# Performance work log

Measured on AMD Instinct MI355X. Metric: run time of the kernel, lower is better.

The kernel has to match this reference:

```python
import jax, jax.numpy as jnp
import numpy as np

B, T, D, H, L, V = 4, 1024, 1024, 16, 12, 8192
DH = D // H
FF = 4 * D


def _ln(x, g, b, eps=1e-5):
    m = x.mean(-1, keepdims=True)
    v = x.var(-1, keepdims=True)
    return (x - m) / jnp.sqrt(v + eps) * g + b


def setup_inputs() -> dict:
    key = jax.random.key(0)
    ks = iter(jax.random.split(key, 32))
    s = 0.02
    inp = {
        "idx": jax.random.randint(next(ks), (B, T), 0, V),
        "tk_emb": jax.random.normal(next(ks), (V, D), jnp.float32) * s,
        "pos_emb": jax.random.normal(next(ks), (V, D), jnp.float32) * s,
        "ln1_g": jnp.ones((L, D)), "ln1_b": jnp.zeros((L, D)),
        "Wq": jax.random.normal(next(ks), (L, H, D, DH), jnp.float32) * s,
        "bq": jnp.zeros((L, H, DH)),
        "Wk": jax.random.normal(next(ks), (L, H, D, DH), jnp.float32) * s,
        "bk": jnp.zeros((L, H, DH)),
        "Wv": jax.random.normal(next(ks), (L, H, D, DH), jnp.float32) * s,
        "bv": jnp.zeros((L, H, DH)),
        "Wo": jax.random.normal(next(ks), (L, D, D), jnp.float32) * s,
        "bo": jnp.zeros((L, D)),
        "ln2_g": jnp.ones((L, D)), "ln2_b": jnp.zeros((L, D)),
        "W1": jax.random.normal(next(ks), (L, D, FF), jnp.float32) * s,
        "b1": jnp.zeros((L, FF)),
        "W2": jax.random.normal(next(ks), (L, FF, D), jnp.float32) * s,
        "b2": jnp.zeros((L, D)),
        "lnf_g": jnp.ones((D,)), "lnf_b": jnp.zeros((D,)),
        "Wout": jax.random.normal(next(ks), (D, V), jnp.float32) * s,
        "bout": jnp.zeros((V,)),
    }
    return inp


def reference(idx, tk_emb, pos_emb, ln1_g, ln1_b, Wq, bq, Wk, bk, Wv, bv,
              Wo, bo, ln2_g, ln2_b, W1, b1, W2, b2, lnf_g, lnf_b, Wout, bout):
    b, t = idx.shape
    x = tk_emb[idx] + pos_emb[:t][None]          # [B,T,D]
    causal = jnp.tril(jnp.ones((t, t), bool))    # [T,T]
    scale = 1.0 / jnp.sqrt(jnp.asarray(DH, x.dtype))

    def block(x, p):
        g1, b1_, wq, bq_, wk, bk_, wv, bv_, wo, bo_, g2, b2_, w1, bb1, w2, bb2 = p
        h = _ln(x, g1, b1_)
        q = jnp.einsum('btd,hde->bhte', h, wq) + bq_[:, None, :]
        k = jnp.einsum('btd,hde->bhte', h, wk) + bk_[:, None, :]
        v = jnp.einsum('btd,hde->bhte', h, wv) + bv_[:, None, :]
        scores = jnp.einsum('bhte,bhse->bhts', q, k) * scale
        scores = jnp.where(causal, scores, jnp.asarray(-jnp.inf, scores.dtype))
        att = jax.nn.softmax(scores, axis=-1)
        o = jnp.einsum('bhts,bhse->bhte', att, v)              # [B,H,T,dh]
        o = o.transpose(0, 2, 1, 3).reshape(x.shape[0], x.shape[1], -1)
        x = x + o @ wo + bo_
        h2 = _ln(x, g2, b2_)
        x = x + jax.nn.gelu(h2 @ w1 + bb1, approximate=False) @ w2 + bb2
        return x, None

    layer_params = (ln1_g, ln1_b, Wq, bq, Wk, bk, Wv, bv, Wo, bo,
                    ln2_g, ln2_b, W1, b1, W2, b2)
    x, _ = jax.lax.scan(block, x, layer_params)
    x = _ln(x, lnf_g, lnf_b)
    logits = x @ Wout + bout
    return logits
```

## Files before the change

### kernel.cpp

```cpp
#include <hip/hip_runtime.h>

#define B_ 4
#define T_ 1024
#define D_ 1024
#define H_ 16
#define DH_ 64
#define L_ 12
#define FF_ 4096
#define V_ 8192
#define M_ 4096

typedef short bf16x8 __attribute__((ext_vector_type(8)));
typedef unsigned short u16x8 __attribute__((ext_vector_type(8)));
typedef unsigned short u16x4 __attribute__((ext_vector_type(4)));
typedef float f32x4 __attribute__((ext_vector_type(4)));

typedef const __attribute__((address_space(1))) void* gas1;
typedef __attribute__((address_space(3))) void* las3;
#define GL2LDS(g, l) __builtin_amdgcn_global_load_lds((gas1)(g), (las3)(l), 16, 0, 0)
#define MFMA16(a, b, c) __builtin_amdgcn_mfma_f32_16x16x32_bf16((a), (b), (c), 0, 0, 0)
#define WVM(n) asm volatile("s_waitcnt vmcnt(" #n ")" ::: "memory")
#define WLG() asm volatile("s_waitcnt lgkmcnt(0)" ::: "memory")
#define BARRIER() asm volatile("s_barrier" ::: "memory")

static __device__ __forceinline__ unsigned short f2bf(float f) {
  unsigned int u = __builtin_bit_cast(unsigned int, f);
  u += 0x7fffu + ((u >> 16) & 1u);
  return (unsigned short)(u >> 16);
}

static __device__ __forceinline__ void xcd_swz(int& bx, int& by) {
  const int gx = gridDim.x;
  const int id = by * gx + bx;
  const int q = (gx * gridDim.y) >> 3;
  const int nid = (id & 7) * q + (id >> 3);
  bx = nid % gx;
  by = nid / gx;
}

static __device__ __forceinline__ void ln_row_store(float4 r, const float* __restrict__ g,
                                                    const float* __restrict__ bb, int row,
                                                    int tid, float* red,
                                                    unsigned short* __restrict__ out) {
  float s = r.x + r.y + r.z + r.w;
  float s2 = r.x * r.x + r.y * r.y + r.z * r.z + r.w * r.w;
#pragma unroll
  for (int off = 32; off; off >>= 1) {
    s += __shfl_down(s, off);
    s2 += __shfl_down(s2, off);
  }
  if ((tid & 63) == 0) { red[tid >> 6] = s; red[4 + (tid >> 6)] = s2; }
  __syncthreads();
  const float ts = red[0] + red[1] + red[2] + red[3];
  const float ts2 = red[4] + red[5] + red[6] + red[7];
  const float mean = ts * (1.f / 1024.f);
  const float var = ts2 * (1.f / 1024.f) - mean * mean;
  const float rstd = rsqrtf(var + 1e-5f);
  const int c = tid * 4;
  u16x4 ov;
  ov[0] = f2bf((r.x - mean) * rstd * g[c] + bb[c]);
  ov[1] = f2bf((r.y - mean) * rstd * g[c + 1] + bb[c + 1]);
  ov[2] = f2bf((r.z - mean) * rstd * g[c + 2] + bb[c + 2]);
  ov[3] = f2bf((r.w - mean) * rstd * g[c + 3] + bb[c + 3]);
  *(u16x4*)&out[(size_t)row * D_ + c] = ov;
}

__global__ __launch_bounds__(256) void embed_ln_kernel(const int* __restrict__ idx,
                                                       const float* __restrict__ tk,
                                                       const float* __restrict__ pe,
                                                       const float* __restrict__ g,
                                                       const float* __restrict__ bb,
                                                       float* __restrict__ x,
                                                       unsigned short* __restrict__ out) {
  __shared__ float red[8];
  const int row = blockIdx.x, tid = threadIdx.x;
  const int t = row & (T_ - 1);
  const int id = idx[row];
  const int c = tid * 4;
  float4 a = *(const float4*)&tk[(size_t)id * D_ + c];
  const float4 p = *(const float4*)&pe[(size_t)t * D_ + c];
  a.x += p.x; a.y += p.y; a.z += p.z; a.w += p.w;
  *(float4*)&x[(size_t)row * D_ + c] = a;
  ln_row_store(a, g, bb, row, tid, red, out);
}

__global__ __launch_bounds__(256) void ln_kernel(const float* __restrict__ x,
                                                 const float* __restrict__ g,
                                                 const float* __restrict__ bb,
                                                 unsigned short* __restrict__ out) {
  __shared__ float red[8];
  const int row = blockIdx.x, tid = threadIdx.x;
  const float4 v = *(const float4*)&x[(size_t)row * D_ + tid * 4];
  ln_row_store(v, g, bb, row, tid, red, out);
}

__global__ __launch_bounds__(256) void redk_ln_kernel(const float* __restrict__ part,
                                                      const float* __restrict__ bias,
                                                      float* __restrict__ x,
                                                      const float* __restrict__ g,
                                                      const float* __restrict__ bb,
                                                      unsigned short* __restrict__ out) {
  __shared__ float red[8];
  const int row = blockIdx.x, tid = threadIdx.x;
  const size_t i = (size_t)row * D_ + tid * 4;
  float4 r = *(const float4*)&x[i];
  const float4 bv = *(const float4*)&bias[tid * 4];
  const size_t stride = (size_t)M_ * D_;
  float4 p0 = *(const float4*)&part[i];
  float4 p1 = *(const float4*)&part[i + stride];
  float4 p2 = *(const float4*)&part[i + 2 * stride];
  float4 p3 = *(const float4*)&part[i + 3 * stride];
  r.x += bv.x + ((p0.x + p1.x) + (p2.x + p3.x));
  r.y += bv.y + ((p0.y + p1.y) + (p2.y + p3.y));
  r.z += bv.z + ((p0.z + p1.z) + (p2.z + p3.z));
  r.w += bv.w + ((p0.w + p1.w) + (p2.w + p3.w));
  *(float4*)&x[i] = r;
  ln_row_store(r, g, bb, row, tid, red, out);
}

__global__ __launch_bounds__(256) void tpose_kernel(const float* __restrict__ in,
                                                    unsigned short* __restrict__ out,
                                                    int R, int C, long in_bs,
                                                    long out_bs_i, int inner, long out_bs_o) {
  __shared__ float tile[64][65];
  const int z = blockIdx.z;
  in += (long)z * in_bs;
  out += (long)(z % inner) * out_bs_i + (long)(z / inner) * out_bs_o;
  const int tx = threadIdx.x, ty = threadIdx.y;
  const int c = blockIdx.x * 64 + tx;
  const int r0 = blockIdx.y * 64;
#pragma unroll
  for (int i = 0; i < 16; i++) tile[ty + i * 4][tx] = in[(long)(r0 + ty + i * 4) * C + c];
  __syncthreads();
  const int oc = blockIdx.y * 64 + tx;
  const int or0 = blockIdx.x * 64;
#pragma unroll
  for (int i = 0; i < 16; i++)
    out[(long)(or0 + ty + i * 4) * R + oc] = f2bf(tile[tx][ty + i * 4]);
}

__global__ void bcat_kernel(const float* __restrict__ bq, const float* __restrict__ bk,
                            const float* __restrict__ bv, float* __restrict__ bqkv) {
  const int l = blockIdx.x;
  for (int i = threadIdx.x; i < 1024; i += 256) {
    bqkv[l * 3072 + i] = bq[l * 1024 + i];
    bqkv[l * 3072 + 1024 + i] = bk[l * 1024 + i];
    bqkv[l * 3072 + 2048 + i] = bv[l * 1024 + i];
  }
}

template <int EPI>
__global__ __launch_bounds__(512, 2) void gemm256(const unsigned short* __restrict__ A,
                                                  const unsigned short* __restrict__ Bt,
                                                  const float* __restrict__ bias,
                                                  void* outp, int Kc, int ld, int N) {
  __shared__ unsigned short lds[65536];
  const int tid = threadIdx.x;
  const int lane = tid & 63, w = tid >> 6;
  const int wm = w >> 2, wn = w & 3;
  const int l15 = lane & 15, lh = lane >> 4;
  int bx = blockIdx.x, by = blockIdx.y;
  xcd_swz(bx, by);
  const int row0 = by * 256, col0 = bx * 256;
  const int z = blockIdx.z;
  const int nt = Kc >> 6;
  const int laneoff = (lh * 8) ^ (((l15 >> 1) & 3) << 3);
  const int cswz = ((tid & 3) * 8) ^ (((tid >> 3) & 3) << 3);
  const unsigned short* gA = A + (size_t)(row0 + (tid >> 2)) * ld + z * Kc + cswz;
  const unsigned short* gB = Bt + (size_t)(col0 + (tid >> 2)) * ld + z * Kc + cswz;
  const size_t rblk = (size_t)128 * ld;
  const int arow = wm * 128 + l15;
  const int brow = wn * 64 + l15;

  f32x4 acc[8][4];
#pragma unroll
  for (int m = 0; m < 8; m++)
#pragma unroll
    for (int n = 0; n < 4; n++) acc[m][n] = f32x4{0.f, 0.f, 0.f, 0.f};

  auto issueA = [&](int t, int r) {
    unsigned short* d = lds + (t & 1) * 32768 + r * 8192 + tid * 8;
    const unsigned short* s = gA + t * 64 + r * 32;
    GL2LDS(s, d);
    GL2LDS(s + rblk, d + 4096);
  };
  auto issueB = [&](int t, int r) {
    unsigned short* d = lds + (t & 1) * 32768 + 16384 + r * 8192 + tid * 8;
    const unsigned short* s = gB + t * 64 + r * 32;
    GL2LDS(s, d);
    GL2LDS(s + rblk, d + 4096);
  };

  issueA(0, 0); issueB(0, 0); issueA(0, 1); issueB(0, 1);
  issueA(1, 0); issueB(1, 0);
  WVM(8);
  BARRIER();

  bf16x8 aF[4], bF[4];
  for (int t = 0; t < nt; ++t) {
    const bool last = (t == nt - 1);
    const unsigned short* ab = lds + (t & 1) * 32768;
    const unsigned short* bb2 = ab + 16384;
#pragma unroll
    for (int m = 0; m < 4; m++) aF[m] = *(const bf16x8*)(ab + (arow + m * 16) * 32 + laneoff);
#pragma unroll
    for (int n = 0; n < 4; n++) bF[n] = *(const bf16x8*)(bb2 + (brow + n * 16) * 32 + laneoff);
    if (!last) issueA(t + 1, 1);
    BARRIER();
    __builtin_amdgcn_s_setprio(1);
#pragma unroll
    for (int m = 0; m < 4; m++)
#pragma unroll
      for (int n = 0; n < 4; n++) acc[m][n] = MFMA16(aF[m], bF[n], acc[m][n]);
    __builtin_amdgcn_s_setprio(0);
    BARRIER();
#pragma unroll
    for (int m = 0; m < 4; m++) aF[m] = *(const bf16x8*)(ab + (arow + (m + 4) * 16) * 32 + laneoff);
    if (!last) issueB(t + 1, 1);
    BARRIER();
    __builtin_amdgcn_s_setprio(1);
#pragma unroll
    for (int m = 0; m < 4; m++)
#pragma unroll
      for (int n = 0; n < 4; n++) acc[m + 4][n] = MFMA16(aF[m], bF[n], acc[m + 4][n]);
    __builtin_amdgcn_s_setprio(0);
    if (last) { WVM(0); } else { WVM(8); }
    BARRIER();
#pragma unroll
    for (int m = 0; m < 4; m++) aF[m] = *(const bf16x8*)(ab + 8192 + (arow + m * 16) * 32 + laneoff);
#pragma unroll
    for (int n = 0; n < 4; n++) bF[n] = *(const bf16x8*)(bb2 + 8192 + (brow + n * 16) * 32 + laneoff);
    if (t + 2 < nt) issueA(t + 2, 0);
    BARRIER();
    __builtin_amdgcn_s_setprio(1);
#pragma unroll
    for (int m = 0; m < 4; m++)
#pragma unroll
      for (int n = 0; n < 4; n++) acc[m][n] = MFMA16(aF[m], bF[n], acc[m][n]);
    __builtin_amdgcn_s_setprio(0);
    BARRIER();
#pragma unroll
    for (int m = 0; m < 4; m++) aF[m] = *(const bf16x8*)(ab + 8192 + (arow + (m + 4) * 16) * 32 + laneoff);
    if (t + 2 < nt) issueB(t + 2, 0);
    BARRIER();
    __builtin_amdgcn_s_setprio(1);
#pragma unroll
    for (int m = 0; m < 4; m++)
#pragma unroll
      for (int n = 0; n < 4; n++) acc[m + 4][n] = MFMA16(aF[m], bF[n], acc[m + 4][n]);
    __builtin_amdgcn_s_setprio(0);
    if (!last) {
      if (t == nt - 2) { WVM(4); } else { WVM(8); }
    }
    BARRIER();
  }

#pragma unroll
  for (int n = 0; n < 4; n++) {
    const int c = col0 + wn * 64 + n * 16 + l15;
    const float bv = (EPI == 4) ? 0.f : bias[c];
#pragma unroll
    for (int m = 0; m < 8; m++) {
      const int r = row0 + wm * 128 + m * 16 + lh * 4;
#pragma unroll
      for (int j = 0; j < 4; j++) {
        float val = acc[m][n][j] + bv;
        const size_t oi = (size_t)(r + j) * N + c;
        if constexpr (EPI == 0) {
          ((unsigned short*)outp)[oi] = f2bf(val);
        } else if constexpr (EPI == 1) {
          val = 0.5f * val * (1.f + erff(val * 0.70710678118654752f));
          ((unsigned short*)outp)[oi] = f2bf(val);
        } else if constexpr (EPI == 4) {
          ((float*)outp)[(size_t)z * ((size_t)gridDim.y * 256) * N + oi] = val;
        } else {
          ((float*)outp)[oi] = val;
        }
      }
    }
  }
}

template <int EPI, int BN, int DEPTH>
__global__ __launch_bounds__(256) void gemmP(const unsigned short* __restrict__ A,
                                             const unsigned short* __restrict__ Bt,
                                             const float* __restrict__ bias,
                                             const float* resid, void* outp,
                                             int K, int N) {
  constexpr int NB = DEPTH + 1;
  constexpr int TILE = (128 + BN) * 32;
  constexpr int NF = BN / 32;
  __shared__ unsigned short lds[NB * TILE];
  const int tid = threadIdx.x;
  const int lane = tid & 63;
  const int w = tid >> 6;
  const int l15 = lane & 15, lh = lane >> 4;
  const int wr = (w >> 1) * 64, wc = (w & 1) * (BN / 2);
  int bx = blockIdx.x, by = blockIdx.y;
  xcd_swz(bx, by);
  const int row0 = by * 128, col0 = bx * BN;

  const unsigned short* gA = A + (size_t)(row0 + (tid >> 2)) * K + (tid & 3) * 8;
  const unsigned short* gB = Bt + (size_t)(col0 + (tid >> 2)) * K + (tid & 3) * 8;
  const size_t rstep = (size_t)64 * K;

  f32x4 acc[4][NF];
#pragma unroll
  for (int m = 0; m < 4; m++)
#pragma unroll
    for (int n = 0; n < NF; n++) acc[m][n] = f32x4{0.f, 0.f, 0.f, 0.f};

  const int nt = K >> 5;

  auto ISSUE = [&](int t) {
    unsigned short* buf = lds + (t % NB) * TILE;
    const unsigned short* a = gA + t * 32;
    GL2LDS(a, buf + tid * 8);
    GL2LDS(a + rstep, buf + 2048 + tid * 8);
    const unsigned short* b = gB + t * 32;
    unsigned short* bb = buf + 128 * 32;
    GL2LDS(b, bb + tid * 8);
    if constexpr (BN == 128) GL2LDS(b + rstep, bb + 2048 + tid * 8);
  };

#pragma unroll
  for (int t = 0; t < DEPTH; t++) ISSUE(t);

  for (int i = 0; i < nt; i++) {
    const int rem = nt - 1 - i;
    if (rem >= DEPTH - 1) {
      if constexpr ((2 + (BN == 128 ? 2 : 1)) * (DEPTH - 1) == 4) WVM(4);
      else WVM(6);
    } else if (DEPTH == 3 && rem == 1) {
      WVM(3);
    } else {
      WVM(0);
    }
    BARRIER();
    const unsigned short* buf = lds + (i % NB) * TILE;
    const unsigned short* rdA = buf + (wr + l15) * 32 + lh * 8;
    const unsigned short* rdB = buf + 128 * 32 + (wc + l15) * 32 + lh * 8;
    bf16x8 aF[4], bF[NF];
#pragma unroll
    for (int m = 0; m < 4; m++) aF[m] = *(const bf16x8*)(rdA + m * 512);
#pragma unroll
    for (int n = 0; n < NF; n++) bF[n] = *(const bf16x8*)(rdB + n * 512);
#pragma unroll
    for (int m = 0; m < 4; m++)
#pragma unroll
      for (int n = 0; n < NF; n++) acc[m][n] = MFMA16(aF[m], bF[n], acc[m][n]);
    if (i + DEPTH < nt) ISSUE(i + DEPTH);
  }

#pragma unroll
  for (int n = 0; n < NF; n++) {
    const int c = col0 + wc + n * 16 + l15;
    const float bv = bias[c];
#pragma unroll
    for (int m = 0; m < 4; m++) {
      const int r = row0 + wr + m * 16 + lh * 4;
#pragma unroll
      for (int j = 0; j < 4; j++) {
        float val = acc[m][n][j] + bv;
        const size_t oi = (size_t)(r + j) * N + c;
        if constexpr (EPI == 0) {
          ((unsigned short*)outp)[oi] = f2bf(val);
        } else if constexpr (EPI == 1) {
          val = 0.5f * val * (1.f + erff(val * 0.70710678118654752f));
          ((unsigned short*)outp)[oi] = f2bf(val);
        } else if constexpr (EPI == 2) {
          ((float*)outp)[oi] = resid[oi] + val;
        } else {
          ((float*)outp)[oi] = val;
        }
      }
    }
  }
}

__global__ __launch_bounds__(512) void attn_kernel(const unsigned short* __restrict__ qkv,
                                                   unsigned short* __restrict__ o) {
  __shared__ unsigned short Ks[2][64 * 72];
  __shared__ unsigned short Vts[2][64 * 72];
  __shared__ unsigned short Ps[8][16 * 72];
  const int tid = threadIdx.x;
  const int lane = tid & 63, w = tid >> 6;
  const int l15 = lane & 15, lh = lane >> 4;
  const int qt = blockIdx.x;
  const int bh = blockIdx.y;
  const int b = bh >> 4, h = bh & 15;
  const int rb = b * T_;
  const int q0 = qt * 128;
  const int nkt = 2 * qt + 2;

  bf16x8 qf[2];
  {
    const unsigned short* qp = qkv + (size_t)(rb + q0 + w * 16 + l15) * 3072 + h * 64 + lh * 8;
    qf[0] = *(const bf16x8*)qp;
    qf[1] = *(const bf16x8*)(qp + 32);
  }
  f32x4 oa[4];
  float mrun[4], lrun[4];
#pragma unroll
  for (int n = 0; n < 4; n++) oa[n] = f32x4{0.f, 0.f, 0.f, 0.f};
#pragma unroll
  for (int j = 0; j < 4; j++) { mrun[j] = -1e30f; lrun[j] = 0.f; }

  const int row_l = w * 16 + lh * 4;

  u16x8 kreg, vreg;
  auto loadKV = [&](int kt) {
    kreg = *(const u16x8*)(qkv + (size_t)(rb + kt * 64 + (tid >> 3)) * 3072 + 1024 + h * 64 +
                           (tid & 7) * 8);
    vreg = *(const u16x8*)(qkv + (size_t)(rb + kt * 64 + lane) * 3072 + 2048 + h * 64 + w * 8);
  };
  auto writeKV = [&](int kt) {
    const int bs = kt & 1;
    *(u16x8*)&Ks[bs][(tid >> 3) * 72 + (tid & 7) * 8] = kreg;
#pragma unroll
    for (int j = 0; j < 8; j++) Vts[bs][(w * 8 + j) * 72 + lane] = vreg[j];
  };

  loadKV(0);
  WVM(0);
  writeKV(0);
  loadKV(1);
  WLG();
  BARRIER();

  for (int kt = 0; kt < nkt; ++kt) {
    const int bs = kt & 1;
    f32x4 sa[4];
#pragma unroll
    for (int n = 0; n < 4; n++) sa[n] = f32x4{0.f, 0.f, 0.f, 0.f};
    __builtin_amdgcn_s_setprio(1);
#pragma unroll
    for (int ke = 0; ke < 2; ke++) {
#pragma unroll
      for (int n = 0; n < 4; n++) {
        const bf16x8 kf = *(const bf16x8*)&Ks[bs][(n * 16 + l15) * 72 + ke * 32 + lh * 8];
        sa[n] = MFMA16(qf[ke], kf, sa[n]);
      }
    }
    __builtin_amdgcn_s_setprio(0);
    float sv[4][4];
    const bool diag = (kt >= 2 * qt);
#pragma unroll
    for (int n = 0; n < 4; n++) {
      const int colv = kt * 64 + n * 16 + l15;
#pragma unroll
      for (int j = 0; j < 4; j++) {
        float v = sa[n][j] * 0.125f;
        if (diag && colv > q0 + row_l + j) v = -1e30f;
        sv[n][j] = v;
      }
    }
    float mx[4];
#pragma unroll
    for (int j = 0; j < 4; j++)
      mx[j] = fmaxf(fmaxf(sv[0][j], sv[1][j]), fmaxf(sv[2][j], sv[3][j]));
#pragma unroll
    for (int off = 1; off < 16; off <<= 1)
#pragma unroll
      for (int j = 0; j < 4; j++) mx[j] = fmaxf(mx[j], __shfl_xor(mx[j], off));
    float corr[4], rs[4];
#pragma unroll
    for (int j = 0; j < 4; j++) {
      const float m2 = fmaxf(mrun[j], mx[j]);
      corr[j] = __expf(mrun[j] - m2);
      mrun[j] = m2;
      rs[j] = 0.f;
    }
#pragma unroll
    for (int n = 0; n < 4; n++)
#pragma unroll
      for (int j = 0; j < 4; j++) {
        const float p = __expf(sv[n][j] - mrun[j]);
        rs[j] += p;
        Ps[w][(lh * 4 + j) * 72 + n * 16 + l15] = f2bf(p);
      }
#pragma unroll
    for (int off = 1; off < 16; off <<= 1)
#pragma unroll
      for (int j = 0; j < 4; j++) rs[j] += __shfl_xor(rs[j], off);
#pragma unroll
    for (int j = 0; j < 4; j++) lrun[j] = lrun[j] * corr[j] + rs[j];
#pragma unroll
    for (int n = 0; n < 4; n++)
#pragma unroll
      for (int j = 0; j < 4; j++) oa[n][j] *= corr[j];
    __builtin_amdgcn_s_setprio(1);
#pragma unroll
    for (int ks = 0; ks < 2; ks++) {
      const bf16x8 pf = *(const bf16x8*)&Ps[w][l15 * 72 + ks * 32 + lh * 8];
#pragma unroll
      for (int n = 0; n < 4; n++) {
        const bf16x8 vf = *(const bf16x8*)&Vts[bs][(n * 16 + l15) * 72 + ks * 32 + lh * 8];
        oa[n] = MFMA16(pf, vf, oa[n]);
      }
    }
    __builtin_amdgcn_s_setprio(0);
    if (kt + 1 < nkt) {
      WVM(0);
      writeKV(kt + 1);
      if (kt + 2 < nkt) loadKV(kt + 2);
      WLG();
      BARRIER();
    }
  }
#pragma unroll
  for (int n = 0; n < 4; n++)
#pragma unroll
    for (int j = 0; j < 4; j++) {
      o[(size_t)(rb + q0 + row_l + j) * D_ + h * 64 + n * 16 + l15] =
          f2bf(oa[n][j] / lrun[j]);
    }
}

extern "C" void kernel_launch(void* const* d_in, const int* in_sizes, int n_in,
                              void* d_out, int out_size, void* d_ws, size_t ws_size,
                              hipStream_t stream) {
  const int* idx = (const int*)d_in[0];
  const float* tk = (const float*)d_in[1];
  const float* pe = (const float*)d_in[2];
  const float* ln1g = (const float*)d_in[3];
  const float* ln1b = (const float*)d_in[4];
  const float* Wq = (const float*)d_in[5];
  const float* bq = (const float*)d_in[6];
  const float* Wk = (const float*)d_in[7];
  const float* bk = (const float*)d_in[8];
  const float* Wv = (const float*)d_in[9];
  const float* bv = (const float*)d_in[10];
  const float* Wo = (const float*)d_in[11];
  const float* bo = (const float*)d_in[12];
  const float* ln2g = (const float*)d_in[13];
  const float* ln2b = (const float*)d_in[14];
  const float* W1 = (const float*)d_in[15];
  const float* b1 = (const float*)d_in[16];
  const float* W2 = (const float*)d_in[17];
  const float* b2 = (const float*)d_in[18];
  const float* lnfg = (const float*)d_in[19];
  const float* lnfb = (const float*)d_in[20];
  const float* Wout = (const float*)d_in[21];
  const float* bout = (const float*)d_in[22];

  char* ws = (char*)d_ws;
  size_t off = 0;
  auto alloc = [&](size_t bytes) {
    void* p = ws + off;
    off += (bytes + 255) & ~(size_t)255;
    return p;
  };
  unsigned short* wqkv = (unsigned short*)alloc(12ull * 3072 * 1024 * 2);
  unsigned short* wo = (unsigned short*)alloc(12ull * 1024 * 1024 * 2);
  unsigned short* w1 = (unsigned short*)alloc(12ull * 4096 * 1024 * 2);
  unsigned short* w2 = (unsigned short*)alloc(12ull * 4096 * 1024 * 2);
  unsigned short* wout = (unsigned short*)alloc(8192ull * 1024 * 2);
  float* bqkv = (float*)alloc(12ull * 3072 * 4);
  float* x = (float*)alloc(4096ull * 1024 * 4);
  unsigned short* hb = (unsigned short*)alloc(4096ull * 1024 * 2);
  unsigned short* qkvb = (unsigned short*)alloc(4096ull * 3072 * 2);
  unsigned short* ob = (unsigned short*)alloc(4096ull * 1024 * 2);
  unsigned short* ub = (unsigned short*)alloc(4096ull * 4096 * 2);
  float* part = (float*)alloc(4ull * 4096 * 1024 * 4);

  const dim3 tb(64, 4);
  tpose_kernel<<<dim3(1, 16, 192), tb, 0, stream>>>(Wq, wqkv, 1024, 64, 65536, 65536, 16, 3145728);
  tpose_kernel<<<dim3(1, 16, 192), tb, 0, stream>>>(Wk, wqkv + 1024 * 1024, 1024, 64, 65536, 65536, 16, 3145728);
  tpose_kernel<<<dim3(1, 16, 192), tb, 0, stream>>>(Wv, wqkv + 2048 * 1024, 1024, 64, 65536, 65536, 16, 3145728);
  tpose_kernel<<<dim3(16, 16, 12), tb, 0, stream>>>(Wo, wo, 1024, 1024, 1048576, 0, 1, 1048576);
  tpose_kernel<<<dim3(64, 16, 12), tb, 0, stream>>>(W1, w1, 1024, 4096, 4194304, 0, 1, 4194304);
  tpose_kernel<<<dim3(16, 64, 12), tb, 0, stream>>>(W2, w2, 4096, 1024, 4194304, 0, 1, 4194304);
  tpose_kernel<<<dim3(128, 16, 1), tb, 0, stream>>>(Wout, wout, 1024, 8192, 0, 0, 1, 0);
  bcat_kernel<<<12, 256, 0, stream>>>(bq, bk, bv, bqkv);
  embed_ln_kernel<<<4096, 256, 0, stream>>>(idx, tk, pe, ln1g, ln1b, x, hb);

  for (int l = 0; l < 12; l++) {
    gemmP<0, 128, 2><<<dim3(24, 32), 256, 0, stream>>>(hb, wqkv + (size_t)l * 3145728,
                                                       bqkv + l * 3072, nullptr, qkvb, 1024, 3072);
    attn_kernel<<<dim3(8, 64), 512, 0, stream>>>(qkvb, ob);
    gemmP<2, 64, 3><<<dim3(16, 32), 256, 0, stream>>>(ob, wo + (size_t)l * 1048576,
                                                      bo + l * 1024, x, x, 1024, 1024);
    ln_kernel<<<4096, 256, 0, stream>>>(x, ln2g + l * 1024, ln2b + l * 1024, hb);
    gemm256<1><<<dim3(16, 16), 512, 0, stream>>>(hb, w1 + (size_t)l * 4194304,
                                                 b1 + l * 4096, ub, 1024, 1024, 4096);
    gemm256<4><<<dim3(4, 16, 4), 512, 0, stream>>>(ub, w2 + (size_t)l * 4194304,
                                                   nullptr, part, 1024, 4096, 1024);
    const float* ng = (l < 11) ? (ln1g + (l + 1) * 1024) : lnfg;
    const float* nb = (l < 11) ? (ln1b + (l + 1) * 1024) : lnfb;
    redk_ln_kernel<<<4096, 256, 0, stream>>>(part, b2 + l * 1024, x, ng, nb, hb);
  }
  gemm256<3><<<dim3(32, 16), 512, 0, stream>>>(hb, wout, bout, d_out, 1024, 1024, 8192);
}
```

Before: 3.098 ms.

## Store split-K partials in bf16, prescale Q, lazy softmax rescale, reverse attention tiles

The W2 split-K GEMM now writes its partial sums as bf16 instead of fp32, which halves the write and read traffic of the reduction buffer feeding redk_ln. The attention kernel folds the 1/sqrt(dh) scale into Q once at load. It skips the online-softmax rescale of the output accumulator when the row max grows by at most 8, and it schedules the longest causal query tiles first. These changes reduce memory traffic and per-tile ALU work at the cost of extra bf16 rounding in the residual stream and in Q.

```diff
diff --git a/kernel.cpp b/kernel.cpp
--- a/kernel.cpp
+++ b/kernel.cpp
@@ -27,6 +27,10 @@
   unsigned int u = __builtin_bit_cast(unsigned int, f);
   u += 0x7fffu + ((u >> 16) & 1u);
   return (unsigned short)(u >> 16);
+}
+static __device__ __forceinline__ float bf2f(unsigned short u) {
+  unsigned int v = (unsigned int)u << 16;
+  return __builtin_bit_cast(float, v);
 }
 
 static __device__ __forceinline__ void xcd_swz(int& bx, int& by) {
@@ -94,7 +98,7 @@
   ln_row_store(v, g, bb, row, tid, red, out);
 }
 
-__global__ __launch_bounds__(256) void redk_ln_kernel(const float* __restrict__ part,
+__global__ __launch_bounds__(256) void redk_ln_kernel(const unsigned short* __restrict__ part,
                                                       const float* __restrict__ bias,
                                                       float* __restrict__ x,
                                                       const float* __restrict__ g,
@@ -106,14 +110,14 @@
   float4 r = *(const float4*)&x[i];
   const float4 bv = *(const float4*)&bias[tid * 4];
   const size_t stride = (size_t)M_ * D_;
-  float4 p0 = *(const float4*)&part[i];
-  float4 p1 = *(const float4*)&part[i + stride];
-  float4 p2 = *(const float4*)&part[i + 2 * stride];
-  float4 p3 = *(const float4*)&part[i + 3 * stride];
-  r.x += bv.x + ((p0.x + p1.x) + (p2.x + p3.x));
-  r.y += bv.y + ((p0.y + p1.y) + (p2.y + p3.y));
-  r.z += bv.z + ((p0.z + p1.z) + (p2.z + p3.z));
-  r.w += bv.w + ((p0.w + p1.w) + (p2.w + p3.w));
+  const u16x4 q0 = *(const u16x4*)&part[i];
+  const u16x4 q1 = *(const u16x4*)&part[i + stride];
+  const u16x4 q2 = *(const u16x4*)&part[i + 2 * stride];
+  const u16x4 q3 = *(const u16x4*)&part[i + 3 * stride];
+  r.x += bv.x + ((bf2f(q0[0]) + bf2f(q1[0])) + (bf2f(q2[0]) + bf2f(q3[0])));
+  r.y += bv.y + ((bf2f(q0[1]) + bf2f(q1[1])) + (bf2f(q2[1]) + bf2f(q3[1])));
+  r.z += bv.z + ((bf2f(q0[2]) + bf2f(q1[2])) + (bf2f(q2[2]) + bf2f(q3[2])));
+  r.w += bv.w + ((bf2f(q0[3]) + bf2f(q1[3])) + (bf2f(q2[3]) + bf2f(q3[3])));
   *(float4*)&x[i] = r;
   ln_row_store(r, g, bb, row, tid, red, out);
 }
@@ -258,7 +262,7 @@
 #pragma unroll
   for (int n = 0; n < 4; n++) {
     const int c = col0 + wn * 64 + n * 16 + l15;
-    const float bv = (EPI == 4) ? 0.f : bias[c];
+    const float bv = (EPI == 5) ? 0.f : bias[c];
 #pragma unroll
     for (int m = 0; m < 8; m++) {
       const int r = row0 + wm * 128 + m * 16 + lh * 4;
@@ -271,8 +275,8 @@
         } else if constexpr (EPI == 1) {
           val = 0.5f * val * (1.f + erff(val * 0.70710678118654752f));
           ((unsigned short*)outp)[oi] = f2bf(val);
-        } else if constexpr (EPI == 4) {
-          ((float*)outp)[(size_t)z * ((size_t)gridDim.y * 256) * N + oi] = val;
+        } else if constexpr (EPI == 5) {
+          ((unsigned short*)outp)[(size_t)z * ((size_t)gridDim.y * 256) * N + oi] = f2bf(val);
         } else {
           ((float*)outp)[oi] = val;
         }
@@ -386,7 +390,7 @@
   const int tid = threadIdx.x;
   const int lane = tid & 63, w = tid >> 6;
   const int l15 = lane & 15, lh = lane >> 4;
-  const int qt = blockIdx.x;
+  const int qt = gridDim.x - 1 - blockIdx.x;
   const int bh = blockIdx.y;
   const int b = bh >> 4, h = bh & 15;
   const int rb = b * T_;
@@ -398,6 +402,13 @@
     const unsigned short* qp = qkv + (size_t)(rb + q0 + w * 16 + l15) * 3072 + h * 64 + lh * 8;
     qf[0] = *(const bf16x8*)qp;
     qf[1] = *(const bf16x8*)(qp + 32);
+#pragma unroll
+    for (int e = 0; e < 2; e++) {
+      u16x8 u = __builtin_bit_cast(u16x8, qf[e]);
+#pragma unroll
+      for (int j = 0; j < 8; j++) u[j] = f2bf(bf2f(u[j]) * 0.125f);
+      qf[e] = __builtin_bit_cast(bf16x8, u);
+    }
   }
   f32x4 oa[4];
   float mrun[4], lrun[4];
@@ -450,7 +461,7 @@
       const int colv = kt * 64 + n * 16 + l15;
 #pragma unroll
       for (int j = 0; j < 4; j++) {
-        float v = sa[n][j] * 0.125f;
+        float v = sa[n][j];
         if (diag && colv > q0 + row_l + j) v = -1e30f;
         sv[n][j] = v;
       }
@@ -463,14 +474,26 @@
     for (int off = 1; off < 16; off <<= 1)
 #pragma unroll
       for (int j = 0; j < 4; j++) mx[j] = fmaxf(mx[j], __shfl_xor(mx[j], off));
-    float corr[4], rs[4];
-#pragma unroll
-    for (int j = 0; j < 4; j++) {
-      const float m2 = fmaxf(mrun[j], mx[j]);
-      corr[j] = __expf(mrun[j] - m2);
-      mrun[j] = m2;
-      rs[j] = 0.f;
-    }
+    bool small = true;
+#pragma unroll
+    for (int j = 0; j < 4; j++) small = small && (mx[j] - mrun[j] <= 8.f);
+    if (!__all(small)) {
+      float corr[4];
+#pragma unroll
+      for (int j = 0; j < 4; j++) {
+        const float m2 = fmaxf(mrun[j], mx[j]);
+        corr[j] = __expf(mrun[j] - m2);
+        mrun[j] = m2;
+        lrun[j] *= corr[j];
+      }
+#pragma unroll
+      for (int n = 0; n < 4; n++)
+#pragma unroll
+        for (int j = 0; j < 4; j++) oa[n][j] *= corr[j];
+    }
+    float rs[4];
+#pragma unroll
+    for (int j = 0; j < 4; j++) rs[j] = 0.f;
 #pragma unroll
     for (int n = 0; n < 4; n++)
 #pragma unroll
@@ -484,11 +507,7 @@
 #pragma unroll
       for (int j = 0; j < 4; j++) rs[j] += __shfl_xor(rs[j], off);
 #pragma unroll
-    for (int j = 0; j < 4; j++) lrun[j] = lrun[j] * corr[j] + rs[j];
-#pragma unroll
-    for (int n = 0; n < 4; n++)
-#pragma unroll
-      for (int j = 0; j < 4; j++) oa[n][j] *= corr[j];
+    for (int j = 0; j < 4; j++) lrun[j] += rs[j];
     __builtin_amdgcn_s_setprio(1);
 #pragma unroll
     for (int ks = 0; ks < 2; ks++) {
@@ -562,7 +581,7 @@
   unsigned short* qkvb = (unsigned short*)alloc(4096ull * 3072 * 2);
   unsigned short* ob = (unsigned short*)alloc(4096ull * 1024 * 2);
   unsigned short* ub = (unsigned short*)alloc(4096ull * 4096 * 2);
-  float* part = (float*)alloc(4ull * 4096 * 1024 * 4);
+  unsigned short* part = (unsigned short*)alloc(4ull * 4096 * 1024 * 2);
 
   const dim3 tb(64, 4);
   tpose_kernel<<<dim3(1, 16, 192), tb, 0, stream>>>(Wq, wqkv, 1024, 64, 65536, 65536, 16, 3145728);
@@ -584,7 +603,7 @@
     ln_kernel<<<4096, 256, 0, stream>>>(x, ln2g + l * 1024, ln2b + l * 1024, hb);
     gemm256<1><<<dim3(16, 16), 512, 0, stream>>>(hb, w1 + (size_t)l * 4194304,
                                                  b1 + l * 4096, ub, 1024, 1024, 4096);
-    gemm256<4><<<dim3(4, 16, 4), 512, 0, stream>>>(ub, w2 + (size_t)l * 4194304,
+    gemm256<5><<<dim3(4, 16, 4), 512, 0, stream>>>(ub, w2 + (size_t)l * 4194304,
                                                    nullptr, part, 1024, 4096, 1024);
     const float* ng = (l < 11) ? (ln1g + (l + 1) * 1024) : lnfg;
     const float* nb = (l < 11) ? (ln1b + (l + 1) * 1024) : lnfb;
```

New measurement: 3.094 ms. About the same (-0.2%).
